# Kernel tuning notes

Measured on AMD Instinct MI355X. Metric: run time of the kernel, lower is better.

The kernel has to match this reference:

```python
import jax, jax.numpy as jnp
import numpy as np

N_HEAD = 16
N_KV_HEAD = 4
HEAD_DIM = 64
ROPE_THETA = 10000.0
EPS = 1e-6


def _rope_cos_sin(T, D, theta):
    # matches torch: freqs_cis[t, i] = exp(1j * t * theta**(-2i/D)), i in [0, D//2)
    inv_freq = theta ** (-jnp.arange(0, D, 2, dtype=jnp.float32) / D)  # [D//2]
    freqs = jnp.arange(T, dtype=jnp.float32)[:, None] * inv_freq[None, :]  # [T, D//2]
    return jnp.cos(freqs), jnp.sin(freqs)


def _apply_rope(x, cos, sin):
    # x: [B, T, H, D]; pairs are (even, odd) along last dim, complex-multiplied by freqs_cis
    B, T, H, D = x.shape
    xr = x.reshape(B, T, H, D // 2, 2)
    xe, xo = xr[..., 0], xr[..., 1]
    c = cos[None, :, None, :]  # [1, T, 1, D//2]
    s = sin[None, :, None, :]
    oe = xe * c - xo * s
    oo = xe * s + xo * c
    return jnp.stack([oe, oo], axis=-1).reshape(B, T, H, D)


def _qk_norm(x):
    rms = jnp.sqrt(jnp.mean(x * x, axis=-1, keepdims=True) + EPS)
    return x / rms


def setup_inputs() -> dict:
    key = jax.random.key(0)
    k = jax.random.split(key, 5)
    B, T, C = 4, 2048, 1024
    sc = 1.0 / np.sqrt(C)
    return {
        "x": jax.random.normal(k[0], (B, T, C), jnp.float32),
        "wq": jax.random.normal(k[1], (N_HEAD * HEAD_DIM, C), jnp.float32) * sc,
        "wk": jax.random.normal(k[2], (N_KV_HEAD * HEAD_DIM, C), jnp.float32) * sc,
        "wv": jax.random.normal(k[3], (N_KV_HEAD * HEAD_DIM, C), jnp.float32) * sc,
        "wo": jax.random.normal(k[4], (C, N_HEAD * HEAD_DIM), jnp.float32) * sc,
    }


def reference(x, wq, wk, wv, wo):
    B, T, C = x.shape
    H, KVH, D = N_HEAD, N_KV_HEAD, HEAD_DIM
    n_rep = H // KVH

    q = (x @ wq.T).reshape(B, T, H, D)
    k = (x @ wk.T).reshape(B, T, KVH, D)
    v = (x @ wv.T).reshape(B, T, KVH, D)

    cos, sin = _rope_cos_sin(T, D, ROPE_THETA)
    q = _qk_norm(_apply_rope(q, cos, sin))
    k = _qk_norm(_apply_rope(k, cos, sin))

    # GQA expand kv heads to n_head
    k = jnp.repeat(k, n_rep, axis=2)  # [B, T, H, D]
    v = jnp.repeat(v, n_rep, axis=2)

    q = q.transpose(0, 2, 1, 3)  # [B, H, T, D]
    k = k.transpose(0, 2, 1, 3)
    v = v.transpose(0, 2, 1, 3)

    scale = 1.0 / np.sqrt(D)
    scores = jnp.einsum("bhqd,bhkd->bhqk", q, k) * scale
    causal = jnp.tril(jnp.ones((T, T), dtype=bool))
    scores = jnp.where(causal[None, None], scores, -jnp.inf)
    attn = jax.nn.softmax(scores, axis=-1)
    y = jnp.einsum("bhqk,bhkd->bhqd", attn, v)  # [B, H, T, D]
    y = y.transpose(0, 2, 1, 3).reshape(B, T, H * D)
    return y @ wo.T
```

## Files before the change

### kernel.cpp

```cpp
#include <hip/hip_runtime.h>
#include <hip/hip_bf16.h>

typedef __attribute__((ext_vector_type(8))) __bf16 bf16x8;
typedef __attribute__((ext_vector_type(2))) float f32x2;
typedef __attribute__((ext_vector_type(4))) float f32x4;
typedef __attribute__((ext_vector_type(16))) float f32x16;

#define MFMA16(a, b, c) __builtin_amdgcn_mfma_f32_16x16x32_bf16((a), (b), (c), 0, 0, 0)
#define MFMA32(a, b, c) __builtin_amdgcn_mfma_f32_32x32x16_bf16((a), (b), (c), 0, 0, 0)

template <bool B> struct BoolC { static constexpr bool value = B; };

__device__ __forceinline__ unsigned short f2bf(float f) {
    unsigned u = __builtin_bit_cast(unsigned, f);
    u = (u + 0x7fffu + ((u >> 16) & 1u)) >> 16;
    return (unsigned short)u;
}

__device__ __forceinline__ unsigned cvt_pk_bf16(float lo, float hi) {
    unsigned r;
    asm("v_cvt_pk_bf16_f32 %0, %1, %2" : "=v"(r) : "v"(lo), "v"(hi));
    return r;
}

__device__ __forceinline__ void permswap(unsigned& a, unsigned& b) {
    asm("v_permlane32_swap_b32 %0, %1" : "+v"(a), "+v"(b));
}

__device__ __forceinline__ void gll16(const void* g, void* l) {
    __builtin_amdgcn_global_load_lds((const __attribute__((address_space(1))) void*)g,
                                     (__attribute__((address_space(3))) void*)l, 16, 0, 0);
}

__global__ __launch_bounds__(256) void cvt_f32_bf16(const float4* __restrict__ in,
                                                    ushort4* __restrict__ out, int n4) {
    int i = blockIdx.x * 256 + threadIdx.x;
    if (i >= n4) return;
    float4 v = in[i];
    ushort4 o;
    o.x = f2bf(v.x); o.y = f2bf(v.y); o.z = f2bf(v.z); o.w = f2bf(v.w);
    out[i] = o;
}

__global__ __launch_bounds__(256) void trig_table(float2* __restrict__ tbl) {
    int i = blockIdx.x * 256 + threadIdx.x;
    int t = i >> 5, j = i & 31;
    float inv = powf(10000.0f, -(float)(2 * j) * (1.0f / 64.0f));
    float a = (float)t * inv;
    tbl[i] = make_float2(cosf(a), sinf(a));
}

__global__ __launch_bounds__(256) void gemm_bt(const unsigned short* __restrict__ A,
                                               const unsigned short* __restrict__ Bt,
                                               float* __restrict__ C, int M, int N, int K) {
    __shared__ unsigned short As[2][128 * 32];
    __shared__ unsigned short Bs[2][128 * 32];
    const int tid = threadIdx.x;
    const int wid = tid >> 6, lane = tid & 63;
    const size_t brow = (size_t)blockIdx.x * 128, bcol = (size_t)blockIdx.y * 128;
    const int nkt = K >> 5;

    auto stage = [&](int buf, int kt) {
#pragma unroll
        for (int j = 0; j < 2; ++j) {
            int e = (j * 256 + tid) * 8;
            int r = e >> 5, c = e & 31;
            gll16(A + (brow + r) * K + kt * 32 + c, &As[buf][e]);
        }
#pragma unroll
        for (int j = 0; j < 2; ++j) {
            int e = (j * 256 + tid) * 8;
            int r = e >> 5, c = e & 31;
            gll16(Bt + (bcol + r) * K + kt * 32 + c, &Bs[buf][e]);
        }
    };

    f32x4 acc[4][4] = {};
    const int wm = (wid >> 1) * 64, wn = (wid & 1) * 64;
    const int fr = lane & 15, fk = (lane >> 4) * 8;

    stage(0, 0);
    for (int kt = 0; kt < nkt; ++kt) {
        __syncthreads();
        if (kt + 1 < nkt) stage((kt + 1) & 1, kt + 1);
        const int buf = kt & 1;
        bf16x8 af[4], bfr[4];
#pragma unroll
        for (int i = 0; i < 4; ++i)
            af[i] = *(const bf16x8*)&As[buf][(wm + i * 16 + fr) * 32 + fk];
#pragma unroll
        for (int i = 0; i < 4; ++i)
            bfr[i] = *(const bf16x8*)&Bs[buf][(wn + i * 16 + fr) * 32 + fk];
#pragma unroll
        for (int i = 0; i < 4; ++i)
#pragma unroll
            for (int j = 0; j < 4; ++j)
                acc[i][j] = MFMA16(af[i], bfr[j], acc[i][j]);
    }

    const int orow = (lane >> 4) * 4, ocol = lane & 15;
#pragma unroll
    for (int i = 0; i < 4; ++i)
#pragma unroll
        for (int j = 0; j < 4; ++j)
#pragma unroll
            for (int r = 0; r < 4; ++r)
                C[(brow + wm + i * 16 + orow + r) * N + (bcol + wn + j * 16 + ocol)] =
                    acc[i][j][r];
}

__global__ __launch_bounds__(256) void rope_norm(const float* __restrict__ qkv,
                                                 const float2* __restrict__ tbl,
                                                 unsigned short* __restrict__ qb,
                                                 unsigned short* __restrict__ kb,
                                                 unsigned short* __restrict__ vb) {
    int unit = blockIdx.x * 4 + (threadIdx.x >> 6);
    int lane = threadIdx.x & 63;
    int row = unit / 24;
    int hh = unit - row * 24;
    int b = row >> 11, t = row & 2047;
    int col = (hh < 16) ? hh * 64 : (hh < 20 ? 1024 + (hh - 16) * 64 : 1280 + (hh - 20) * 64);
    float x = qkv[(size_t)row * 1536 + col + lane];
    float o = x;
    if (hh < 20) {
        float partner = __shfl_xor(x, 1);
        float2 cs = tbl[t * 32 + (lane >> 1)];
        float sgn = (lane & 1) ? cs.y : -cs.y;
        o = x * cs.x + partner * sgn;
        float ss = o * o;
#pragma unroll
        for (int off = 1; off < 64; off <<= 1) ss += __shfl_xor(ss, off);
        o = o * rsqrtf(ss * (1.0f / 64.0f) + 1e-6f);
        if (hh < 16) o *= 0.125f;
    }
    unsigned short ob = f2bf(o);
    if (hh < 16)
        qb[(((size_t)(b * 16 + hh)) * 2048 + t) * 64 + lane] = ob;
    else if (hh < 20)
        kb[(((size_t)(b * 4 + (hh - 16))) * 2048 + t) * 64 + lane] = ob;
    else
        vb[(((size_t)(b * 4 + (hh - 20))) * 2048 + t) * 64 + lane] = ob;
}

__global__ __launch_bounds__(256) void vtrans(const unsigned short* __restrict__ vb,
                                              unsigned short* __restrict__ vt) {
    __shared__ unsigned short tile[64][72];
    int bk = blockIdx.y, t0 = blockIdx.x * 64;
    int i = threadIdx.x >> 2, c0 = (threadIdx.x & 3) * 16;
    const unsigned short* src = vb + ((size_t)bk * 2048 + t0) * 64;
#pragma unroll
    for (int j = 0; j < 16; ++j) tile[i][c0 + j] = src[i * 64 + c0 + j];
    __syncthreads();
    unsigned short* dst = vt + (size_t)bk * 64 * 2048 + (size_t)i * 2048 + t0 + c0;
#pragma unroll
    for (int j = 0; j < 16; ++j) dst[j] = tile[c0 + j][i];
}

__global__ __launch_bounds__(256) void attn_fwd(const unsigned short* __restrict__ qb,
                                                const unsigned short* __restrict__ kbuf,
                                                const unsigned short* __restrict__ vt,
                                                float* __restrict__ accOg,
                                                float* __restrict__ accLg) {
    int orig = blockIdx.x;
    int wg = (orig & 7) * 320 + (orig >> 3);
    int bh = wg / 40;
    int u = 39 - (wg - bh * 40);
    int qt, ci, nc;
    if (u < 4)       { qt = u;               ci = 0;            nc = 1; }
    else if (u < 12) { qt = 4 + ((u - 4) >> 1);  ci = (u - 4) & 1;  nc = 2; }
    else if (u < 24) { qt = 8 + (u - 12) / 3;    ci = (u - 12) % 3; nc = 3; }
    else             { qt = 12 + ((u - 24) >> 2); ci = (u - 24) & 3; nc = 4; }
    const int nkt = 2 * qt + 2;
    const int t0 = ci * nkt / nc, t1 = (ci + 1) * nkt / nc;
    const int qbase = qt * 128;

    int b = bh >> 4, h = bh & 15, kvh = h >> 2;
    int tid = threadIdx.x, wid = tid >> 6, lane = tid & 63;
    int qrow0 = qbase + wid * 32;
    const unsigned short* Q = qb + ((size_t)(b * 16 + h)) * 2048 * 64;
    const unsigned short* Kp = kbuf + ((size_t)(b * 4 + kvh)) * 2048 * 64;
    const unsigned short* Vp = vt + ((size_t)(b * 4 + kvh)) * 64 * 2048;
    const int q32 = lane & 31, hi = lane >> 5;
    const int swz = (q32 & 7) ^ ((q32 >> 3) & 3);

    __shared__ unsigned short Klds[2][4096];
    __shared__ unsigned short Vlds[2][4096];

    auto stage = [&](int buf, int kt) {
#pragma unroll
        for (int j = 0; j < 2; ++j) {
            int t = j * 256 + tid;
            int k = t >> 3, c = (t & 7) ^ (k & 7) ^ ((k >> 3) & 3);
            gll16(Kp + ((size_t)(kt * 64 + k)) * 64 + c * 8, &Klds[buf][t * 8]);
        }
#pragma unroll
        for (int j = 0; j < 2; ++j) {
            int t = j * 256 + tid;
            int d = t >> 3, c = (t & 7) ^ (d & 7) ^ ((d >> 3) & 3);
            gll16(Vp + (size_t)d * 2048 + kt * 64 + c * 8, &Vlds[buf][t * 8]);
        }
    };

    bf16x8 qf[4];
#pragma unroll
    for (int kd = 0; kd < 4; ++kd)
        qf[kd] = *(const bf16x8*)&Q[(qrow0 + q32) * 64 + kd * 16 + hi * 8];

    f32x16 accO[2] = {};
    f32x2 lr2 = {0.0f, 0.0f};

    stage(0, t0);
    for (int kt = t0; kt < t1; ++kt) {
        __syncthreads();
        if (kt + 1 < t1) stage((kt + 1 - t0) & 1, kt + 1);
        const int cur = (kt - t0) & 1;
        const int kb0 = kt * 64;
        if (kb0 <= qrow0 + 31) {
            f32x16 s[2] = {};
#pragma unroll
            for (int j = 0; j < 2; ++j) {
                int row = j * 32 + q32;
#pragma unroll
                for (int kd = 0; kd < 4; ++kd) {
                    bf16x8 kf = *(const bf16x8*)&Klds[cur][row * 64 + ((2 * kd + hi) ^ swz) * 8];
                    s[j] = MFMA32(kf, qf[kd], s[j]);
                }
            }
            const int qg = qrow0 + q32;
            bf16x8 pf[4];
            auto build = [&](auto mc) {
                constexpr bool MASKED = decltype(mc)::value;
#pragma unroll
                for (int j = 0; j < 2; ++j) {
                    float p[16];
#pragma unroll
                    for (int r = 0; r < 16; ++r) {
                        float v = __builtin_exp2f(fmaf(s[j][r], 1.44269504f, -11.54156036f));
                        if (MASKED) {
                            int key = kb0 + j * 32 + (r & 3) + 8 * (r >> 2) + 4 * hi;
                            if (key > qg) v = 0.0f;
                        }
                        p[r] = v;
                    }
#pragma unroll
                    for (int i = 0; i < 8; ++i) {
                        f32x2 pp = {p[2 * i], p[2 * i + 1]};
                        asm("v_pk_add_f32 %0, %0, %1" : "+v"(lr2) : "v"(pp));
                    }
#pragma unroll
                    for (int kl = 0; kl < 2; ++kl) {
                        unsigned c0 = cvt_pk_bf16(p[8 * kl + 0], p[8 * kl + 1]);
                        unsigned c1 = cvt_pk_bf16(p[8 * kl + 4], p[8 * kl + 5]);
                        unsigned c2 = cvt_pk_bf16(p[8 * kl + 2], p[8 * kl + 3]);
                        unsigned c3 = cvt_pk_bf16(p[8 * kl + 6], p[8 * kl + 7]);
                        permswap(c0, c1);
                        permswap(c2, c3);
                        union { bf16x8 v; unsigned u[4]; } pk;
                        pk.u[0] = c0; pk.u[1] = c2; pk.u[2] = c1; pk.u[3] = c3;
                        pf[j * 2 + kl] = pk.v;
                    }
                }
            };
            if (kb0 + 63 > qrow0) build(BoolC<true>{});
            else                  build(BoolC<false>{});
#pragma unroll
            for (int nd = 0; nd < 2; ++nd) {
                int row = nd * 32 + q32;
#pragma unroll
                for (int ks = 0; ks < 4; ++ks) {
                    bf16x8 vf = *(const bf16x8*)&Vlds[cur][row * 64 + ((2 * ks + hi) ^ swz) * 8];
                    accO[nd] = MFMA32(pf[ks], vf, accO[nd]);
                }
            }
        }
    }

    float lrun = lr2[0] + lr2[1];
    unsigned lu = __builtin_bit_cast(unsigned, lrun);
    unsigned la = lu, lb = lu;
    permswap(la, lb);
    float L = __builtin_bit_cast(float, la) + __builtin_bit_cast(float, lb);

    if (t0 * 64 <= qrow0 + 31) {
#pragma unroll
        for (int nd = 0; nd < 2; ++nd)
#pragma unroll
            for (int r = 0; r < 16; ++r) {
                int rowq = qrow0 + (r & 3) + 8 * (r >> 2) + 4 * hi;
                atomicAdd(accOg + ((size_t)bh * 2048 + rowq) * 64 + nd * 32 + q32, accO[nd][r]);
            }
        if (lane < 32) atomicAdd(accLg + (size_t)bh * 2048 + qrow0 + q32, L);
    }
}

__global__ __launch_bounds__(256) void attn_fin(const float* __restrict__ accOg,
                                                const float* __restrict__ accLg,
                                                unsigned short* __restrict__ y) {
    int idx = blockIdx.x * 256 + threadIdx.x;
    int dg = idx & 15;
    int row = idx >> 4;
    int bh = row >> 11, t = row & 2047;
    int b = bh >> 4, h = bh & 15;
    f32x4 o = *(const f32x4*)&accOg[(size_t)row * 64 + dg * 4];
    float inv = 1.0f / accLg[row];
    ushort4 w;
    w.x = f2bf(o[0] * inv); w.y = f2bf(o[1] * inv);
    w.z = f2bf(o[2] * inv); w.w = f2bf(o[3] * inv);
    *(ushort4*)&y[((size_t)(b * 2048 + t)) * 1024 + h * 64 + dg * 4] = w;
}

extern "C" void kernel_launch(void* const* d_in, const int* in_sizes, int n_in,
                              void* d_out, int out_size, void* d_ws, size_t ws_size,
                              hipStream_t stream) {
    const float* x = (const float*)d_in[0];
    const float* wq = (const float*)d_in[1];
    const float* wk = (const float*)d_in[2];
    const float* wv = (const float*)d_in[3];
    const float* wo = (const float*)d_in[4];
    float* out = (float*)d_out;

    char* ws = (char*)d_ws;
    size_t off = 0;
    auto alloc = [&](size_t bytes) {
        void* p = ws + off;
        off += (bytes + 255) & ~(size_t)255;
        return p;
    };
    unsigned short* xb    = (unsigned short*)alloc(8192ull * 1024 * 2);
    unsigned short* wqkvb = (unsigned short*)alloc(1536ull * 1024 * 2);
    unsigned short* wob   = (unsigned short*)alloc(1024ull * 1024 * 2);
    float*          qkv   = (float*)alloc(8192ull * 1536 * 4);
    float2*         tbl   = (float2*)alloc(2048ull * 32 * 8);
    unsigned short* qb    = (unsigned short*)alloc(8192ull * 1024 * 2);
    unsigned short* kb    = (unsigned short*)alloc(4ull * 4 * 2048 * 64 * 2);
    unsigned short* vb    = (unsigned short*)alloc(4ull * 4 * 2048 * 64 * 2);
    unsigned short* vt    = (unsigned short*)alloc(4ull * 4 * 64 * 2048 * 2);

    float*          accO  = qkv;
    float*          accL  = qkv + 64ull * 2048 * 64;
    unsigned short* ybf   = xb;

    cvt_f32_bf16<<<(2097152 + 255) / 256, 256, 0, stream>>>((const float4*)x, (ushort4*)xb, 2097152);
    cvt_f32_bf16<<<(262144 + 255) / 256, 256, 0, stream>>>((const float4*)wq, (ushort4*)wqkvb, 262144);
    cvt_f32_bf16<<<(65536 + 255) / 256, 256, 0, stream>>>((const float4*)wk, (ushort4*)(wqkvb + 1048576), 65536);
    cvt_f32_bf16<<<(65536 + 255) / 256, 256, 0, stream>>>((const float4*)wv, (ushort4*)(wqkvb + 1310720), 65536);
    cvt_f32_bf16<<<(262144 + 255) / 256, 256, 0, stream>>>((const float4*)wo, (ushort4*)wob, 262144);

    trig_table<<<256, 256, 0, stream>>>(tbl);

    gemm_bt<<<dim3(64, 12), 256, 0, stream>>>(xb, wqkvb, qkv, 8192, 1536, 1024);

    rope_norm<<<(8192 * 24) / 4, 256, 0, stream>>>(qkv, tbl, qb, kb, vb);

    vtrans<<<dim3(32, 16), 256, 0, stream>>>(vb, vt);

    hipMemsetAsync(accO, 0, (64ull * 2048 * 64 + 64ull * 2048) * 4, stream);

    attn_fwd<<<2560, 256, 0, stream>>>(qb, kb, vt, accO, accL);

    attn_fin<<<8192, 256, 0, stream>>>(accO, accL, ybf);

    gemm_bt<<<dim3(64, 8), 256, 0, stream>>>(ybf, wob, out, 8192, 1024, 1024);
}
```

Before: 214.6 us.

## Fuse conversion kernels, emit bf16 QKV, triple-buffer attention and fold softmax scale

Merges the five f32-to-bf16 conversions and the trig table into one launch. The QKV GEMM now writes bf16 output, and rope_norm and vtrans read that directly, which drops the separate V copy and halves the intermediate traffic. The attention kernel moves to three-stage K/V buffering with explicit vmcnt waits and s_setprio around the MFMA blocks. It also folds log2(e) and the max offset into the Q scale and the score initial value, which removes an FMA per score. The risks are precision loss from rounding QKV to bf16 before norm/rope and extra LDS per block that may lower occupancy.

```diff
diff --git a/kernel.cpp b/kernel.cpp
--- a/kernel.cpp
+++ b/kernel.cpp
@@ -1,5 +1,6 @@
 #include <hip/hip_runtime.h>
 #include <hip/hip_bf16.h>
+#include <type_traits>
 
 typedef __attribute__((ext_vector_type(8))) __bf16 bf16x8;
 typedef __attribute__((ext_vector_type(2))) float f32x2;
@@ -17,6 +18,10 @@
     return (unsigned short)u;
 }
 
+__device__ __forceinline__ float bf2f(unsigned short u) {
+    return __builtin_bit_cast(float, (unsigned)u << 16);
+}
+
 __device__ __forceinline__ unsigned cvt_pk_bf16(float lo, float hi) {
     unsigned r;
     asm("v_cvt_pk_bf16_f32 %0, %1, %2" : "=v"(r) : "v"(lo), "v"(hi));
@@ -32,27 +37,40 @@
                                      (__attribute__((address_space(3))) void*)l, 16, 0, 0);
 }
 
-__global__ __launch_bounds__(256) void cvt_f32_bf16(const float4* __restrict__ in,
-                                                    ushort4* __restrict__ out, int n4) {
+__global__ __launch_bounds__(256) void cvt_fused(const float4* __restrict__ x,
+                                                 const float4* __restrict__ wq,
+                                                 const float4* __restrict__ wk,
+                                                 const float4* __restrict__ wv,
+                                                 const float4* __restrict__ wo,
+                                                 ushort4* __restrict__ xb,
+                                                 ushort4* __restrict__ wqkvb,
+                                                 ushort4* __restrict__ wob,
+                                                 float2* __restrict__ tbl) {
     int i = blockIdx.x * 256 + threadIdx.x;
-    if (i >= n4) return;
-    float4 v = in[i];
-    ushort4 o;
-    o.x = f2bf(v.x); o.y = f2bf(v.y); o.z = f2bf(v.z); o.w = f2bf(v.w);
-    out[i] = o;
-}
-
-__global__ __launch_bounds__(256) void trig_table(float2* __restrict__ tbl) {
-    int i = blockIdx.x * 256 + threadIdx.x;
-    int t = i >> 5, j = i & 31;
-    float inv = powf(10000.0f, -(float)(2 * j) * (1.0f / 64.0f));
-    float a = (float)t * inv;
-    tbl[i] = make_float2(cosf(a), sinf(a));
-}
-
-__global__ __launch_bounds__(256) void gemm_bt(const unsigned short* __restrict__ A,
-                                               const unsigned short* __restrict__ Bt,
-                                               float* __restrict__ C, int M, int N, int K) {
+    if (i < 2752512) {
+        const float4* src; ushort4* dst; int j;
+        if (i < 2097152)      { src = x;  dst = xb;             j = i; }
+        else if (i < 2359296) { src = wq; dst = wqkvb;          j = i - 2097152; }
+        else if (i < 2424832) { src = wk; dst = wqkvb + 262144; j = i - 2359296; }
+        else if (i < 2490368) { src = wv; dst = wqkvb + 327680; j = i - 2424832; }
+        else                  { src = wo; dst = wob;            j = i - 2490368; }
+        float4 v = src[j];
+        ushort4 o;
+        o.x = f2bf(v.x); o.y = f2bf(v.y); o.z = f2bf(v.z); o.w = f2bf(v.w);
+        dst[j] = o;
+    } else {
+        int j = i - 2752512;
+        int t = j >> 5, k = j & 31;
+        float inv = powf(10000.0f, -(float)(2 * k) * (1.0f / 64.0f));
+        float a = (float)t * inv;
+        tbl[j] = make_float2(cosf(a), sinf(a));
+    }
+}
+
+template <typename OT>
+__global__ __launch_bounds__(256) void gemm_bt_t(const unsigned short* __restrict__ A,
+                                                 const unsigned short* __restrict__ Bt,
+                                                 OT* __restrict__ C, int M, int N, int K) {
     __shared__ unsigned short As[2][128 * 32];
     __shared__ unsigned short Bs[2][128 * 32];
     const int tid = threadIdx.x;
@@ -104,52 +122,51 @@
 #pragma unroll
         for (int j = 0; j < 4; ++j)
 #pragma unroll
-            for (int r = 0; r < 4; ++r)
-                C[(brow + wm + i * 16 + orow + r) * N + (bcol + wn + j * 16 + ocol)] =
-                    acc[i][j][r];
-}
-
-__global__ __launch_bounds__(256) void rope_norm(const float* __restrict__ qkv,
+            for (int r = 0; r < 4; ++r) {
+                size_t idx = (brow + wm + i * 16 + orow + r) * N + (bcol + wn + j * 16 + ocol);
+                if constexpr (std::is_same_v<OT, unsigned short>)
+                    C[idx] = f2bf(acc[i][j][r]);
+                else
+                    C[idx] = acc[i][j][r];
+            }
+}
+
+__global__ __launch_bounds__(256) void rope_norm(const unsigned short* __restrict__ qkvb,
                                                  const float2* __restrict__ tbl,
                                                  unsigned short* __restrict__ qb,
-                                                 unsigned short* __restrict__ kb,
-                                                 unsigned short* __restrict__ vb) {
+                                                 unsigned short* __restrict__ kb) {
     int unit = blockIdx.x * 4 + (threadIdx.x >> 6);
     int lane = threadIdx.x & 63;
-    int row = unit / 24;
-    int hh = unit - row * 24;
+    int row = unit / 20;
+    int hh = unit - row * 20;
     int b = row >> 11, t = row & 2047;
-    int col = (hh < 16) ? hh * 64 : (hh < 20 ? 1024 + (hh - 16) * 64 : 1280 + (hh - 20) * 64);
-    float x = qkv[(size_t)row * 1536 + col + lane];
-    float o = x;
-    if (hh < 20) {
-        float partner = __shfl_xor(x, 1);
-        float2 cs = tbl[t * 32 + (lane >> 1)];
-        float sgn = (lane & 1) ? cs.y : -cs.y;
-        o = x * cs.x + partner * sgn;
-        float ss = o * o;
-#pragma unroll
-        for (int off = 1; off < 64; off <<= 1) ss += __shfl_xor(ss, off);
-        o = o * rsqrtf(ss * (1.0f / 64.0f) + 1e-6f);
-        if (hh < 16) o *= 0.125f;
-    }
+    int col = (hh < 16) ? hh * 64 : 1024 + (hh - 16) * 64;
+    float x = bf2f(qkvb[(size_t)row * 1536 + col + lane]);
+    float partner = __shfl_xor(x, 1);
+    float2 cs = tbl[t * 32 + (lane >> 1)];
+    float sgn = (lane & 1) ? cs.y : -cs.y;
+    float o = x * cs.x + partner * sgn;
+    float ss = o * o;
+#pragma unroll
+    for (int off = 1; off < 64; off <<= 1) ss += __shfl_xor(ss, off);
+    o = o * rsqrtf(ss * (1.0f / 64.0f) + 1e-6f);
+    if (hh < 16) o *= 0.18033688f;
     unsigned short ob = f2bf(o);
     if (hh < 16)
         qb[(((size_t)(b * 16 + hh)) * 2048 + t) * 64 + lane] = ob;
-    else if (hh < 20)
+    else
         kb[(((size_t)(b * 4 + (hh - 16))) * 2048 + t) * 64 + lane] = ob;
-    else
-        vb[(((size_t)(b * 4 + (hh - 20))) * 2048 + t) * 64 + lane] = ob;
-}
-
-__global__ __launch_bounds__(256) void vtrans(const unsigned short* __restrict__ vb,
+}
+
+__global__ __launch_bounds__(256) void vtrans(const unsigned short* __restrict__ qkvb,
                                               unsigned short* __restrict__ vt) {
     __shared__ unsigned short tile[64][72];
     int bk = blockIdx.y, t0 = blockIdx.x * 64;
+    int b = bk >> 2, kvh = bk & 3;
     int i = threadIdx.x >> 2, c0 = (threadIdx.x & 3) * 16;
-    const unsigned short* src = vb + ((size_t)bk * 2048 + t0) * 64;
-#pragma unroll
-    for (int j = 0; j < 16; ++j) tile[i][c0 + j] = src[i * 64 + c0 + j];
+    const unsigned short* src = qkvb + ((size_t)(b * 2048 + t0)) * 1536 + 1280 + kvh * 64;
+#pragma unroll
+    for (int j = 0; j < 16; ++j) tile[i][c0 + j] = src[(size_t)i * 1536 + c0 + j];
     __syncthreads();
     unsigned short* dst = vt + (size_t)bk * 64 * 2048 + (size_t)i * 2048 + t0 + c0;
 #pragma unroll
@@ -183,8 +200,8 @@
     const int q32 = lane & 31, hi = lane >> 5;
     const int swz = (q32 & 7) ^ ((q32 >> 3) & 3);
 
-    __shared__ unsigned short Klds[2][4096];
-    __shared__ unsigned short Vlds[2][4096];
+    __shared__ unsigned short Klds[3][4096];
+    __shared__ unsigned short Vlds[3][4096];
 
     auto stage = [&](int buf, int kt) {
 #pragma unroll
@@ -208,15 +225,24 @@
 
     f32x16 accO[2] = {};
     f32x2 lr2 = {0.0f, 0.0f};
-
+    f32x16 s0v;
+#pragma unroll
+    for (int i = 0; i < 16; ++i) s0v[i] = -11.54156036f;
+
+    const int nt = t1 - t0;
     stage(0, t0);
+    if (nt > 1) stage(1, t0 + 1);
+    int cur = 0;
     for (int kt = t0; kt < t1; ++kt) {
-        __syncthreads();
-        if (kt + 1 < t1) stage((kt + 1 - t0) & 1, kt + 1);
-        const int cur = (kt - t0) & 1;
+        if (kt + 1 < t1) { asm volatile("s_waitcnt vmcnt(4)" ::: "memory"); }
+        else             { asm volatile("s_waitcnt vmcnt(0)" ::: "memory"); }
+        __builtin_amdgcn_sched_barrier(0);
+        __builtin_amdgcn_s_barrier();
+        if (kt + 2 < t1) stage(cur == 0 ? 2 : cur - 1, kt + 2);
         const int kb0 = kt * 64;
         if (kb0 <= qrow0 + 31) {
-            f32x16 s[2] = {};
+            f32x16 s[2] = {s0v, s0v};
+            __builtin_amdgcn_s_setprio(1);
 #pragma unroll
             for (int j = 0; j < 2; ++j) {
                 int row = j * 32 + q32;
@@ -226,6 +252,7 @@
                     s[j] = MFMA32(kf, qf[kd], s[j]);
                 }
             }
+            __builtin_amdgcn_s_setprio(0);
             const int qg = qrow0 + q32;
             bf16x8 pf[4];
             auto build = [&](auto mc) {
@@ -235,7 +262,7 @@
                     float p[16];
 #pragma unroll
                     for (int r = 0; r < 16; ++r) {
-                        float v = __builtin_exp2f(fmaf(s[j][r], 1.44269504f, -11.54156036f));
+                        float v = __builtin_exp2f(s[j][r]);
                         if (MASKED) {
                             int key = kb0 + j * 32 + (r & 3) + 8 * (r >> 2) + 4 * hi;
                             if (key > qg) v = 0.0f;
@@ -263,6 +290,7 @@
             };
             if (kb0 + 63 > qrow0) build(BoolC<true>{});
             else                  build(BoolC<false>{});
+            __builtin_amdgcn_s_setprio(1);
 #pragma unroll
             for (int nd = 0; nd < 2; ++nd) {
                 int row = nd * 32 + q32;
@@ -272,7 +300,9 @@
                     accO[nd] = MFMA32(pf[ks], vf, accO[nd]);
                 }
             }
-        }
+            __builtin_amdgcn_s_setprio(0);
+        }
+        cur = (cur == 2) ? 0 : cur + 1;
     }
 
     float lrun = lr2[0] + lr2[1];
@@ -329,30 +359,26 @@
     unsigned short* xb    = (unsigned short*)alloc(8192ull * 1024 * 2);
     unsigned short* wqkvb = (unsigned short*)alloc(1536ull * 1024 * 2);
     unsigned short* wob   = (unsigned short*)alloc(1024ull * 1024 * 2);
-    float*          qkv   = (float*)alloc(8192ull * 1536 * 4);
+    char*           big   = (char*)alloc((64ull * 2048 * 64 + 64ull * 2048) * 4);
     float2*         tbl   = (float2*)alloc(2048ull * 32 * 8);
     unsigned short* qb    = (unsigned short*)alloc(8192ull * 1024 * 2);
     unsigned short* kb    = (unsigned short*)alloc(4ull * 4 * 2048 * 64 * 2);
-    unsigned short* vb    = (unsigned short*)alloc(4ull * 4 * 2048 * 64 * 2);
     unsigned short* vt    = (unsigned short*)alloc(4ull * 4 * 64 * 2048 * 2);
 
-    float*          accO  = qkv;
-    float*          accL  = qkv + 64ull * 2048 * 64;
+    unsigned short* qkvb  = (unsigned short*)big;
+    float*          accO  = (float*)big;
+    float*          accL  = accO + 64ull * 2048 * 64;
     unsigned short* ybf   = xb;
 
-    cvt_f32_bf16<<<(2097152 + 255) / 256, 256, 0, stream>>>((const float4*)x, (ushort4*)xb, 2097152);
-    cvt_f32_bf16<<<(262144 + 255) / 256, 256, 0, stream>>>((const float4*)wq, (ushort4*)wqkvb, 262144);
-    cvt_f32_bf16<<<(65536 + 255) / 256, 256, 0, stream>>>((const float4*)wk, (ushort4*)(wqkvb + 1048576), 65536);
-    cvt_f32_bf16<<<(65536 + 255) / 256, 256, 0, stream>>>((const float4*)wv, (ushort4*)(wqkvb + 1310720), 65536);
-    cvt_f32_bf16<<<(262144 + 255) / 256, 256, 0, stream>>>((const float4*)wo, (ushort4*)wob, 262144);
-
-    trig_table<<<256, 256, 0, stream>>>(tbl);
-
-    gemm_bt<<<dim3(64, 12), 256, 0, stream>>>(xb, wqkvb, qkv, 8192, 1536, 1024);
-
-    rope_norm<<<(8192 * 24) / 4, 256, 0, stream>>>(qkv, tbl, qb, kb, vb);
-
-    vtrans<<<dim3(32, 16), 256, 0, stream>>>(vb, vt);
+    cvt_fused<<<11008, 256, 0, stream>>>((const float4*)x, (const float4*)wq, (const float4*)wk,
+                                         (const float4*)wv, (const float4*)wo,
+                                         (ushort4*)xb, (ushort4*)wqkvb, (ushort4*)wob, tbl);
+
+    gemm_bt_t<unsigned short><<<dim3(64, 12), 256, 0, stream>>>(xb, wqkvb, qkvb, 8192, 1536, 1024);
+
+    rope_norm<<<(8192 * 20) / 4, 256, 0, stream>>>(qkvb, tbl, qb, kb);
+
+    vtrans<<<dim3(32, 16), 256, 0, stream>>>(qkvb, vt);
 
     hipMemsetAsync(accO, 0, (64ull * 2048 * 64 + 64ull * 2048) * 4, stream);
 
@@ -360,5 +386,5 @@
 
     attn_fin<<<8192, 256, 0, stream>>>(accO, accL, ybf);
 
-    gemm_bt<<<dim3(64, 8), 256, 0, stream>>>(ybf, wob, out, 8192, 1024, 1024);
-}
+    gemm_bt_t<float><<<dim3(64, 8), 256, 0, stream>>>(ybf, wob, out, 8192, 1024, 1024);
+}
```

New measurement: 203.7 us. 5.1% less time.
